# Kernel optimization log

Hardware: AMD Instinct MI355X
Metric: run time of the kernel (lower is better)

## Reference

```python
import jax, jax.numpy as jnp
import numpy as np

N = 200000
E = 200000
H = 256
NEG_INF = -1e30


def setup_inputs() -> dict:
    key = jax.random.key(0)
    k1, k2, k3, k4, k5, k6, k7 = jax.random.split(key, 7)
    node_tokens = jax.random.normal(k1, (N, H), dtype=jnp.float32)
    relation_tokens = jax.random.normal(k2, (E, H), dtype=jnp.float32)
    edge_index = jax.random.randint(k3, (2, E), 0, N, dtype=jnp.int64)
    node_is_cvt = jax.random.randint(k4, (N,), 0, 2) > 0
    # learned params (randomized for a non-trivial test; torch inits attn/shared to zeros)
    shared_cvt = jax.random.normal(k5, (H,), dtype=jnp.float32) * 0.02
    attn_vector = jax.random.normal(k6, (H,), dtype=jnp.float32) * 0.1
    W_msg = jax.random.normal(k7, (H, 2 * H), dtype=jnp.float32) * (1.0 / np.sqrt(2 * H))  # torch Linear weight [out,in]
    return {"node_tokens": node_tokens, "relation_tokens": relation_tokens,
            "edge_index": edge_index, "node_is_cvt": node_is_cvt,
            "shared_cvt": shared_cvt, "attn_vector": attn_vector, "W_msg": W_msg}


def reference(node_tokens, relation_tokens, edge_index, node_is_cvt, shared_cvt, attn_vector, W_msg):
    num_nodes, hidden = node_tokens.shape
    num_edges = relation_tokens.shape[0]
    tails = edge_index[1]                      # [E]
    cvt_mask = node_is_cvt.astype(bool)        # [N]
    edge_mask = cvt_mask[tails]                # [E] edges whose tail is a CVT node

    # faithful quirk: nbr token for edge i is node_tokens[i] (edge slot index)
    nbr = node_tokens[:num_edges]                                   # [E, H]
    msg = jnp.concatenate([relation_tokens, nbr], axis=-1) @ W_msg.T  # [E, H]

    # per-edge logits, segment-wise (per tail node) softmax over CVT-tail edges only
    logits = jnp.where(edge_mask, jnp.einsum('eh,h->e', msg, attn_vector), NEG_INF)
    m = jax.ops.segment_max(logits, tails, num_segments=num_nodes)   # [N]
    p = jnp.where(edge_mask, jnp.exp(logits - m[tails]), 0.0)        # [E]
    denom = jax.ops.segment_sum(p, tails, num_segments=num_nodes)    # [N]
    w = p / jnp.where(denom > 0, denom, 1.0)[tails]                  # [E]

    agg = jax.ops.segment_sum(msg * w[:, None], tails, num_segments=num_nodes)  # [N, H]
    cvt_tokens = agg + shared_cvt
    return jnp.where(cvt_mask[:, None], cvt_tokens, node_tokens)
```

## Files before the change

kernel.cpp:

```cpp
#include <hip/hip_runtime.h>
#include <math.h>

#define H   256
#define H2  512
#define MX  16

typedef __attribute__((ext_vector_type(4))) float f32x4;
typedef __attribute__((ext_vector_type(8))) short short8;

__device__ __forceinline__ short f2bf(float f) {
  unsigned u = __builtin_bit_cast(unsigned, f);
  u = (u + 0x7FFFu + ((u >> 16) & 1u)) >> 16;
  return (short)u;
}

__device__ __forceinline__ void gload_lds16(const void* g, void* l) {
  __builtin_amdgcn_global_load_lds(
      (const __attribute__((address_space(1))) unsigned int*)g,
      (__attribute__((address_space(3))) unsigned int*)l, 16, 0, 0);
}

__global__ void k_init(unsigned* cnt, int* ctrs, int N) {
  int i = blockIdx.x * blockDim.x + threadIdx.x;
  if (i < N) cnt[i] = 0u;
  if (i == 0) { ctrs[0] = 0; }
}

__global__ void k_prep(const int* __restrict__ ei, const int* __restrict__ cvt,
                       const float* __restrict__ W, const float* __restrict__ attn,
                       unsigned* __restrict__ cnt, int* __restrict__ ebuf,
                       float* __restrict__ u, short* __restrict__ Wt, int E) {
  int g = blockIdx.x * blockDim.x + threadIdx.x;
  if (g < E) {
    int tail = ei[E + g];
    if (cvt[tail]) {
      unsigned pos = atomicAdd(cnt + tail, 1u);
      if (pos < MX) ebuf[(size_t)tail * MX + pos] = g;
    }
  }
  if (g < 512) {
    float s = 0.f;
    for (int h = 0; h < H; ++h) s += W[(size_t)h * H2 + g] * attn[h];
    u[g] = s;
  }
  if (g < 16384) {
    int n = g & 255, kb = g >> 8;
    const float* src = W + (size_t)n * H2 + kb * 8;
    f32x4 a = *(const f32x4*)src;
    f32x4 b = *(const f32x4*)(src + 4);
    short8 o;
    o[0]=f2bf(a.x); o[1]=f2bf(a.y); o[2]=f2bf(a.z); o[3]=f2bf(a.w);
    o[4]=f2bf(b.x); o[5]=f2bf(b.y); o[6]=f2bf(b.z); o[7]=f2bf(b.w);
    *(short8*)(Wt + (size_t)(kb * 256 + n) * 8) = o;
  }
}

__global__ void k_slots(const unsigned* __restrict__ cnt, int* __restrict__ ctrs,
                        int* __restrict__ actpk, int N) {
  int n = blockIdx.x * blockDim.x + threadIdx.x;
  int lane = threadIdx.x & 63;
  unsigned c = (n < N) ? cnt[n] : 0u;
  bool active = c > 0u;
  unsigned long long mask = __ballot(active);
  if (!mask) return;
  int rank = __popcll(mask & ((1ull << lane) - 1ull));
  int wcount = __popcll(mask);
  int sbase = 0;
  if (lane == 0) sbase = atomicAdd(ctrs + 0, wcount);
  sbase = __shfl(sbase, 0);
  if (active) {
    int cc = (int)(c > MX ? MX : c);
    actpk[sbase + rank] = n | (cc << 20);
  }
}

__global__ __launch_bounds__(256) void k_fin(
    const float* __restrict__ NT, const int* __restrict__ cvt,
    const unsigned* __restrict__ cnt, const float* __restrict__ sc,
    const float* __restrict__ R, const float* __restrict__ u,
    const int* __restrict__ actpk, const int* __restrict__ ctrs,
    const int* __restrict__ ebuf, float* __restrict__ out, int N) {
  int wid = blockIdx.x * 4 + (threadIdx.x >> 6);
  int nw = gridDim.x * 4;
  int lane = threadIdx.x & 63;

  auto outinit = [&]() {
    f32x4 scl = ((const f32x4*)sc)[lane];
    for (int row = wid; row < N; row += nw) {
      int cv = cvt[row];
      if (cv && cnt[row] > 0u) continue;
      f32x4 v = cv ? scl : ((const f32x4*)NT)[(size_t)row * 64 + lane];
      ((f32x4*)out)[(size_t)row * 64 + lane] = v;
    }
  };

  auto gather = [&]() {
    int nAct = ctrs[0];
    int loff = lane * 8;
    const float* src0 = (loff < H) ? (R + loff) : (NT + (loff - H));
    const f32x4* u4 = (const f32x4*)u;
    f32x4 ua = u4[lane * 2], ub = u4[lane * 2 + 1];
    int s = wid;
    if (s >= nAct) return;
    int pk = actpk[s];
    int n = pk & 0xFFFFF, c = pk >> 20;
    int id = (lane < c) ? ebuf[(size_t)n * MX + lane] : 0;
    while (true) {
      int s2 = s + nw;
      int n2 = 0, c2 = 0, id2 = 0;
      if (s2 < nAct) {
        int pk2 = actpk[s2];
        n2 = pk2 & 0xFFFFF; c2 = pk2 >> 20;
        id2 = (lane < c2) ? ebuf[(size_t)n2 * MX + lane] : 0;
      }
      f32x4 x0, x1;
      if (c == 1) {
        int e = __shfl(id, 0);
        const f32x4* src = (const f32x4*)(src0 + (size_t)e * H);
        x0 = src[0]; x1 = src[1];
      } else if (c == 2) {
        int e0 = __shfl(id, 0), e1 = __shfl(id, 1);
        const f32x4* sA = (const f32x4*)(src0 + (size_t)e0 * H);
        const f32x4* sB = (const f32x4*)(src0 + (size_t)e1 * H);
        f32x4 a0 = sA[0], b0 = sA[1], a1 = sB[0], b1 = sB[1];
        float d0 = a0.x*ua.x + a0.y*ua.y + a0.z*ua.z + a0.w*ua.w
                 + b0.x*ub.x + b0.y*ub.y + b0.z*ub.z + b0.w*ub.w;
        float d1 = a1.x*ua.x + a1.y*ua.y + a1.z*ua.z + a1.w*ua.w
                 + b1.x*ub.x + b1.y*ub.y + b1.z*ub.z + b1.w*ub.w;
        #pragma unroll
        for (int off = 32; off > 0; off >>= 1) {
          d0 += __shfl_xor(d0, off);
          d1 += __shfl_xor(d1, off);
        }
        float p0 = __expf(d0), p1 = __expf(d1);
        float inv = 1.f / (p0 + p1);
        p0 *= inv; p1 *= inv;
        x0 = a0 * p0 + a1 * p1;
        x1 = b0 * p0 + b1 * p1;
      } else {
        x0 = (f32x4){0.f,0.f,0.f,0.f}; x1 = x0;
        float den = 0.f;
        for (int i = 0; i < c; ++i) {
          int e = __shfl(id, i);
          const f32x4* src = (const f32x4*)(src0 + (size_t)e * H);
          f32x4 a = src[0], b = src[1];
          float d = a.x*ua.x + a.y*ua.y + a.z*ua.z + a.w*ua.w
                  + b.x*ub.x + b.y*ub.y + b.z*ub.z + b.w*ub.w;
          #pragma unroll
          for (int off = 32; off > 0; off >>= 1) d += __shfl_xor(d, off);
          float pe = __expf(d);
          den += pe;
          x0 += a * pe;
          x1 += b * pe;
        }
        float inv = 1.f / den;
        x0 *= inv; x1 *= inv;
      }
      short8 o;
      o[0]=f2bf(x0.x); o[1]=f2bf(x0.y); o[2]=f2bf(x0.z); o[3]=f2bf(x0.w);
      o[4]=f2bf(x1.x); o[5]=f2bf(x1.y); o[6]=f2bf(x1.z); o[7]=f2bf(x1.w);
      *(short8*)((short*)(out + (size_t)n * H) + loff) = o;
      if (s2 >= nAct) break;
      s = s2; n = n2; c = c2; id = id2;
    }
  };

  if (wid & 1) { gather(); outinit(); }
  else         { outinit(); gather(); }
}

__global__ __launch_bounds__(256) void k_gemm2(
    const short* __restrict__ Wt, const int* __restrict__ actpk,
    const int* __restrict__ ctrs, const float* __restrict__ sc,
    float* __restrict__ out) {
  __shared__ __align__(16) short Bs[2][4][256][8];
  __shared__ __align__(16) short As[2][4][128][8];
  int nAct = ctrs[0];
  int base = blockIdx.x * 128;
  if (base >= nAct) return;
  int tid = threadIdx.x;
  int wave = tid >> 6, lane = tid & 63;
  int l15 = lane & 15, lg = lane >> 4;

  int slot0 = base + lane;       if (slot0 >= nAct) slot0 = nAct - 1;
  int slot1 = base + 64 + lane;  if (slot1 >= nAct) slot1 = nAct - 1;
  const short* arow0 = (const short*)(out + (size_t)(actpk[slot0] & 0xFFFFF) * H);
  const short* arow1 = (const short*)(out + (size_t)(actpk[slot1] & 0xFFFFF) * H);

  auto stage = [&](int b, int kk) {
    gload_lds16(arow0 + kk + wave * 8, &As[b][wave][0][0]);
    gload_lds16(arow1 + kk + wave * 8, &As[b][wave][64][0]);
    int kb = kk >> 3;
    #pragma unroll
    for (int it = 0; it < 4; ++it) {
      const short* src = Wt + (size_t)(kb + it) * 2048 + (size_t)tid * 8;
      gload_lds16(src, &Bs[b][it][wave * 64][0]);
    }
  };

  f32x4 acc[8][4];
  #pragma unroll
  for (int i = 0; i < 8; ++i)
    #pragma unroll
    for (int j = 0; j < 4; ++j) acc[i][j] = (f32x4){0.f, 0.f, 0.f, 0.f};

  stage(0, 0);
  __syncthreads();
  int cur = 0;
  for (int t = 0; t < 16; ++t) {
    if (t < 15) stage(cur ^ 1, (t + 1) * 32);
    short8 bf[4];
    #pragma unroll
    for (int ct = 0; ct < 4; ++ct)
      bf[ct] = *(const short8*)&Bs[cur][lg][wave * 64 + ct * 16 + l15][0];
    #pragma unroll
    for (int rt = 0; rt < 8; ++rt) {
      short8 af = *(const short8*)&As[cur][lg][rt * 16 + l15][0];
      #pragma unroll
      for (int ct = 0; ct < 4; ++ct)
        acc[rt][ct] = __builtin_amdgcn_mfma_f32_16x16x32_bf16(af, bf[ct], acc[rt][ct], 0, 0, 0);
    }
    __syncthreads();
    cur ^= 1;
  }

  #pragma unroll
  for (int rt = 0; rt < 8; ++rt) {
    #pragma unroll
    for (int rr = 0; rr < 4; ++rr) {
      int sD = base + rt * 16 + lg * 4 + rr;
      if (sD >= nAct) continue;
      int n = actpk[sD] & 0xFFFFF;
      float* orow = out + (size_t)n * H;
      #pragma unroll
      for (int ct = 0; ct < 4; ++ct) {
        int c = wave * 64 + ct * 16 + l15;
        __builtin_nontemporal_store(acc[rt][ct][rr] + sc[c], orow + c);
      }
    }
  }
}

extern "C" void kernel_launch(void* const* d_in, const int* in_sizes, int n_in,
                              void* d_out, int out_size, void* d_ws, size_t ws_size,
                              hipStream_t stream) {
  const float* NT   = (const float*)d_in[0];
  const float* R    = (const float*)d_in[1];
  const int*   ei   = (const int*)d_in[2];
  const int*   cvt  = (const int*)d_in[3];
  const float* sc   = (const float*)d_in[4];
  const float* attn = (const float*)d_in[5];
  const float* W    = (const float*)d_in[6];
  float* out = (float*)d_out;

  int N = in_sizes[0] / H;
  int E = in_sizes[1] / H;

  char* wsp = (char*)d_ws;
  auto alloc = [&](size_t bytes) { char* r = wsp; wsp += (bytes + 255) & ~(size_t)255; return r; };
  float*    u       = (float*)alloc(512 * 4);
  short*    Wt      = (short*)alloc((size_t)H * H2 * 2);
  int*      ebuf    = (int*)alloc((size_t)N * MX * 4);
  unsigned* cnt     = (unsigned*)alloc((size_t)N * 4);
  int*      actpk   = (int*)alloc((size_t)N * 4);
  int*      ctrs    = (int*)alloc(2 * 4);

  k_init<<<(N + 255) / 256, 256, 0, stream>>>(cnt, ctrs, N);
  k_prep<<<(E + 255) / 256, 256, 0, stream>>>(ei, cvt, W, attn, cnt, ebuf, u, Wt, E);
  k_slots<<<(N + 255) / 256, 256, 0, stream>>>(cnt, ctrs, actpk, N);
  k_fin<<<2048, 256, 0, stream>>>(NT, cvt, cnt, sc, R, u, actpk, ctrs, ebuf, out, N);
  k_gemm2<<<(N + 127) / 128, 256, 0, stream>>>(Wt, actpk, ctrs, sc, out);
}
```

Before: 208.8 us.

## Fuse attention gather into GEMM via LDS-resident swizzled A tiles

```diff
diff --git a/kernel.cpp b/kernel.cpp
--- a/kernel.cpp
+++ b/kernel.cpp
@@ -4,6 +4,7 @@
 #define H   256
 #define H2  512
 #define MX  16
+#define TR  32
 
 typedef __attribute__((ext_vector_type(4))) float f32x4;
 typedef __attribute__((ext_vector_type(8))) short short8;
@@ -74,148 +75,125 @@
   }
 }
 
-__global__ __launch_bounds__(256) void k_fin(
-    const float* __restrict__ NT, const int* __restrict__ cvt,
-    const unsigned* __restrict__ cnt, const float* __restrict__ sc,
-    const float* __restrict__ R, const float* __restrict__ u,
+__global__ __launch_bounds__(256) void k_gg(
+    const float* __restrict__ R, const float* __restrict__ NT,
+    const short* __restrict__ Wt, const float* __restrict__ u,
     const int* __restrict__ actpk, const int* __restrict__ ctrs,
-    const int* __restrict__ ebuf, float* __restrict__ out, int N) {
-  int wid = blockIdx.x * 4 + (threadIdx.x >> 6);
-  int nw = gridDim.x * 4;
-  int lane = threadIdx.x & 63;
-
-  auto outinit = [&]() {
-    f32x4 scl = ((const f32x4*)sc)[lane];
-    for (int row = wid; row < N; row += nw) {
-      int cv = cvt[row];
-      if (cv && cnt[row] > 0u) continue;
-      f32x4 v = cv ? scl : ((const f32x4*)NT)[(size_t)row * 64 + lane];
-      ((f32x4*)out)[(size_t)row * 64 + lane] = v;
+    const int* __restrict__ ebuf, const float* __restrict__ sc,
+    float* __restrict__ out) {
+  __shared__ __align__(16) short As[TR * 512];
+  __shared__ __align__(16) short Bs[2][4][256][8];
+  __shared__ int nIdx[TR];
+  int nAct = ctrs[0];
+  int base = blockIdx.x * TR;
+  if (base >= nAct) return;
+  int tid = threadIdx.x, wave = tid >> 6, lane = tid & 63;
+  int l15 = lane & 15, lg = lane >> 4;
+
+  auto stageB = [&](int b, int kk) {
+    int kb = kk >> 3;
+    #pragma unroll
+    for (int it = 0; it < 4; ++it) {
+      const short* src = Wt + (size_t)(kb + it) * 2048 + (size_t)tid * 8;
+      gload_lds16(src, &Bs[b][it][wave * 64][0]);
     }
   };
-
-  auto gather = [&]() {
-    int nAct = ctrs[0];
+  stageB(0, 0);
+
+  {
     int loff = lane * 8;
     const float* src0 = (loff < H) ? (R + loff) : (NT + (loff - H));
     const f32x4* u4 = (const f32x4*)u;
     f32x4 ua = u4[lane * 2], ub = u4[lane * 2 + 1];
-    int s = wid;
-    if (s >= nAct) return;
-    int pk = actpk[s];
-    int n = pk & 0xFFFFF, c = pk >> 20;
-    int id = (lane < c) ? ebuf[(size_t)n * MX + lane] : 0;
-    while (true) {
-      int s2 = s + nw;
-      int n2 = 0, c2 = 0, id2 = 0;
-      if (s2 < nAct) {
-        int pk2 = actpk[s2];
-        n2 = pk2 & 0xFFFFF; c2 = pk2 >> 20;
-        id2 = (lane < c2) ? ebuf[(size_t)n2 * MX + lane] : 0;
+    int s0 = base + wave * 8;
+    int nSlots = nAct - s0; if (nSlots > 8) nSlots = 8;
+    if (nSlots > 0) {
+      int myPk = (lane < nSlots) ? actpk[s0 + lane] : 0;
+      int pk = __shfl(myPk, 0);
+      int n = pk & 0xFFFFF, c = pk >> 20;
+      int id = (lane < c) ? ebuf[(size_t)n * MX + lane] : 0;
+      for (int i = 0; i < nSlots; ++i) {
+        int nN = 0, cN = 0, idN = 0;
+        if (i + 1 < nSlots) {
+          int pkN = __shfl(myPk, i + 1);
+          nN = pkN & 0xFFFFF; cN = pkN >> 20;
+          idN = (lane < cN) ? ebuf[(size_t)nN * MX + lane] : 0;
+        }
+        f32x4 x0, x1;
+        if (c == 1) {
+          int e = __shfl(id, 0);
+          const f32x4* src = (const f32x4*)(src0 + (size_t)e * H);
+          x0 = src[0]; x1 = src[1];
+        } else if (c == 2) {
+          int e0 = __shfl(id, 0), e1 = __shfl(id, 1);
+          const f32x4* sA = (const f32x4*)(src0 + (size_t)e0 * H);
+          const f32x4* sB = (const f32x4*)(src0 + (size_t)e1 * H);
+          f32x4 a0 = sA[0], b0 = sA[1], a1 = sB[0], b1 = sB[1];
+          float d0 = a0.x*ua.x + a0.y*ua.y + a0.z*ua.z + a0.w*ua.w
+                   + b0.x*ub.x + b0.y*ub.y + b0.z*ub.z + b0.w*ub.w;
+          float d1 = a1.x*ua.x + a1.y*ua.y + a1.z*ua.z + a1.w*ua.w
+                   + b1.x*ub.x + b1.y*ub.y + b1.z*ub.z + b1.w*ub.w;
+          #pragma unroll
+          for (int off = 32; off > 0; off >>= 1) {
+            d0 += __shfl_xor(d0, off);
+            d1 += __shfl_xor(d1, off);
+          }
+          float p0 = __expf(d0), p1 = __expf(d1);
+          float inv = 1.f / (p0 + p1);
+          p0 *= inv; p1 *= inv;
+          x0 = a0 * p0 + a1 * p1;
+          x1 = b0 * p0 + b1 * p1;
+        } else {
+          x0 = (f32x4){0.f,0.f,0.f,0.f}; x1 = x0;
+          float den = 0.f;
+          for (int j = 0; j < c; ++j) {
+            int e = __shfl(id, j);
+            const f32x4* src = (const f32x4*)(src0 + (size_t)e * H);
+            f32x4 a = src[0], b = src[1];
+            float d = a.x*ua.x + a.y*ua.y + a.z*ua.z + a.w*ua.w
+                    + b.x*ub.x + b.y*ub.y + b.z*ub.z + b.w*ub.w;
+            #pragma unroll
+            for (int off = 32; off > 0; off >>= 1) d += __shfl_xor(d, off);
+            float pe = __expf(d);
+            den += pe;
+            x0 += a * pe;
+            x1 += b * pe;
+          }
+          float inv = 1.f / den;
+          x0 *= inv; x1 *= inv;
+        }
+        short8 o;
+        o[0]=f2bf(x0.x); o[1]=f2bf(x0.y); o[2]=f2bf(x0.z); o[3]=f2bf(x0.w);
+        o[4]=f2bf(x1.x); o[5]=f2bf(x1.y); o[6]=f2bf(x1.z); o[7]=f2bf(x1.w);
+        int r = wave * 8 + i;
+        if (lane == 0) nIdx[r] = n;
+        char* dst = (char*)As + r * 1024 + ((lane * 16) ^ ((r & 7) << 4));
+        *(short8*)dst = o;
+        n = nN; c = cN; id = idN;
       }
-      f32x4 x0, x1;
-      if (c == 1) {
-        int e = __shfl(id, 0);
-        const f32x4* src = (const f32x4*)(src0 + (size_t)e * H);
-        x0 = src[0]; x1 = src[1];
-      } else if (c == 2) {
-        int e0 = __shfl(id, 0), e1 = __shfl(id, 1);
-        const f32x4* sA = (const f32x4*)(src0 + (size_t)e0 * H);
-        const f32x4* sB = (const f32x4*)(src0 + (size_t)e1 * H);
-        f32x4 a0 = sA[0], b0 = sA[1], a1 = sB[0], b1 = sB[1];
-        float d0 = a0.x*ua.x + a0.y*ua.y + a0.z*ua.z + a0.w*ua.w
-                 + b0.x*ub.x + b0.y*ub.y + b0.z*ub.z + b0.w*ub.w;
-        float d1 = a1.x*ua.x + a1.y*ua.y + a1.z*ua.z + a1.w*ua.w
-                 + b1.x*ub.x + b1.y*ub.y + b1.z*ub.z + b1.w*ub.w;
-        #pragma unroll
-        for (int off = 32; off > 0; off >>= 1) {
-          d0 += __shfl_xor(d0, off);
-          d1 += __shfl_xor(d1, off);
-        }
-        float p0 = __expf(d0), p1 = __expf(d1);
-        float inv = 1.f / (p0 + p1);
-        p0 *= inv; p1 *= inv;
-        x0 = a0 * p0 + a1 * p1;
-        x1 = b0 * p0 + b1 * p1;
-      } else {
-        x0 = (f32x4){0.f,0.f,0.f,0.f}; x1 = x0;
-        float den = 0.f;
-        for (int i = 0; i < c; ++i) {
-          int e = __shfl(id, i);
-          const f32x4* src = (const f32x4*)(src0 + (size_t)e * H);
-          f32x4 a = src[0], b = src[1];
-          float d = a.x*ua.x + a.y*ua.y + a.z*ua.z + a.w*ua.w
-                  + b.x*ub.x + b.y*ub.y + b.z*ub.z + b.w*ub.w;
-          #pragma unroll
-          for (int off = 32; off > 0; off >>= 1) d += __shfl_xor(d, off);
-          float pe = __expf(d);
-          den += pe;
-          x0 += a * pe;
-          x1 += b * pe;
-        }
-        float inv = 1.f / den;
-        x0 *= inv; x1 *= inv;
-      }
-      short8 o;
-      o[0]=f2bf(x0.x); o[1]=f2bf(x0.y); o[2]=f2bf(x0.z); o[3]=f2bf(x0.w);
-      o[4]=f2bf(x1.x); o[5]=f2bf(x1.y); o[6]=f2bf(x1.z); o[7]=f2bf(x1.w);
-      *(short8*)((short*)(out + (size_t)n * H) + loff) = o;
-      if (s2 >= nAct) break;
-      s = s2; n = n2; c = c2; id = id2;
-    }
-  };
-
-  if (wid & 1) { gather(); outinit(); }
-  else         { outinit(); gather(); }
-}
-
-__global__ __launch_bounds__(256) void k_gemm2(
-    const short* __restrict__ Wt, const int* __restrict__ actpk,
-    const int* __restrict__ ctrs, const float* __restrict__ sc,
-    float* __restrict__ out) {
-  __shared__ __align__(16) short Bs[2][4][256][8];
-  __shared__ __align__(16) short As[2][4][128][8];
-  int nAct = ctrs[0];
-  int base = blockIdx.x * 128;
-  if (base >= nAct) return;
-  int tid = threadIdx.x;
-  int wave = tid >> 6, lane = tid & 63;
-  int l15 = lane & 15, lg = lane >> 4;
-
-  int slot0 = base + lane;       if (slot0 >= nAct) slot0 = nAct - 1;
-  int slot1 = base + 64 + lane;  if (slot1 >= nAct) slot1 = nAct - 1;
-  const short* arow0 = (const short*)(out + (size_t)(actpk[slot0] & 0xFFFFF) * H);
-  const short* arow1 = (const short*)(out + (size_t)(actpk[slot1] & 0xFFFFF) * H);
-
-  auto stage = [&](int b, int kk) {
-    gload_lds16(arow0 + kk + wave * 8, &As[b][wave][0][0]);
-    gload_lds16(arow1 + kk + wave * 8, &As[b][wave][64][0]);
-    int kb = kk >> 3;
-    #pragma unroll
-    for (int it = 0; it < 4; ++it) {
-      const short* src = Wt + (size_t)(kb + it) * 2048 + (size_t)tid * 8;
-      gload_lds16(src, &Bs[b][it][wave * 64][0]);
-    }
-  };
-
-  f32x4 acc[8][4];
+    }
+  }
+  __syncthreads();
+
+  f32x4 acc[2][4];
   #pragma unroll
-  for (int i = 0; i < 8; ++i)
+  for (int i = 0; i < 2; ++i)
     #pragma unroll
     for (int j = 0; j < 4; ++j) acc[i][j] = (f32x4){0.f, 0.f, 0.f, 0.f};
 
-  stage(0, 0);
-  __syncthreads();
   int cur = 0;
   for (int t = 0; t < 16; ++t) {
-    if (t < 15) stage(cur ^ 1, (t + 1) * 32);
+    if (t < 15) stageB(cur ^ 1, (t + 1) * 32);
+    int kk = t * 32;
     short8 bf[4];
     #pragma unroll
     for (int ct = 0; ct < 4; ++ct)
       bf[ct] = *(const short8*)&Bs[cur][lg][wave * 64 + ct * 16 + l15][0];
     #pragma unroll
-    for (int rt = 0; rt < 8; ++rt) {
-      short8 af = *(const short8*)&As[cur][lg][rt * 16 + l15][0];
+    for (int rt = 0; rt < 2; ++rt) {
+      int row = rt * 16 + l15;
+      short8 af = *(const short8*)((const char*)As + row * 1024 +
+                                   (((kk + lg * 8) * 2) ^ ((row & 7) << 4)));
       #pragma unroll
       for (int ct = 0; ct < 4; ++ct)
         acc[rt][ct] = __builtin_amdgcn_mfma_f32_16x16x32_bf16(af, bf[ct], acc[rt][ct], 0, 0, 0);
@@ -225,12 +203,12 @@
   }
 
   #pragma unroll
-  for (int rt = 0; rt < 8; ++rt) {
+  for (int rt = 0; rt < 2; ++rt) {
     #pragma unroll
     for (int rr = 0; rr < 4; ++rr) {
-      int sD = base + rt * 16 + lg * 4 + rr;
-      if (sD >= nAct) continue;
-      int n = actpk[sD] & 0xFFFFF;
+      int lrow = rt * 16 + lg * 4 + rr;
+      if (base + lrow >= nAct) continue;
+      int n = nIdx[lrow];
       float* orow = out + (size_t)n * H;
       #pragma unroll
       for (int ct = 0; ct < 4; ++ct) {
@@ -238,6 +216,22 @@
         __builtin_nontemporal_store(acc[rt][ct][rr] + sc[c], orow + c);
       }
     }
+  }
+}
+
+__global__ __launch_bounds__(256) void k_out(
+    const float* __restrict__ NT, const int* __restrict__ cvt,
+    const unsigned* __restrict__ cnt, const float* __restrict__ sc,
+    float* __restrict__ out, int N) {
+  int wid = blockIdx.x * 4 + (threadIdx.x >> 6);
+  int nw = gridDim.x * 4;
+  int lane = threadIdx.x & 63;
+  f32x4 scl = ((const f32x4*)sc)[lane];
+  for (int row = wid; row < N; row += nw) {
+    int cv = cvt[row];
+    if (cv && cnt[row] > 0u) continue;
+    f32x4 v = cv ? scl : ((const f32x4*)NT)[(size_t)row * 64 + lane];
+    ((f32x4*)out)[(size_t)row * 64 + lane] = v;
   }
 }
 
@@ -268,6 +262,6 @@
   k_init<<<(N + 255) / 256, 256, 0, stream>>>(cnt, ctrs, N);
   k_prep<<<(E + 255) / 256, 256, 0, stream>>>(ei, cvt, W, attn, cnt, ebuf, u, Wt, E);
   k_slots<<<(N + 255) / 256, 256, 0, stream>>>(cnt, ctrs, actpk, N);
-  k_fin<<<2048, 256, 0, stream>>>(NT, cvt, cnt, sc, R, u, actpk, ctrs, ebuf, out, N);
-  k_gemm2<<<(N + 127) / 128, 256, 0, stream>>>(Wt, actpk, ctrs, sc, out);
-}
+  k_gg<<<(N + TR - 1) / TR, 256, 0, stream>>>(R, NT, Wt, u, actpk, ctrs, ebuf, sc, out);
+  k_out<<<2048, 256, 0, stream>>>(NT, cvt, cnt, sc, out, N);
+}
```

Result: slower. 235.6 us (+12.8%).

## Move output-init pass from gather kernel into GEMM kernel as extra blocks

Applied to the files above, without the earlier changes.

```diff
diff --git a/kernel.cpp b/kernel.cpp
--- a/kernel.cpp
+++ b/kernel.cpp
@@ -74,17 +74,98 @@
   }
 }
 
-__global__ __launch_bounds__(256) void k_fin(
-    const float* __restrict__ NT, const int* __restrict__ cvt,
-    const unsigned* __restrict__ cnt, const float* __restrict__ sc,
-    const float* __restrict__ R, const float* __restrict__ u,
-    const int* __restrict__ actpk, const int* __restrict__ ctrs,
-    const int* __restrict__ ebuf, float* __restrict__ out, int N) {
+__global__ __launch_bounds__(256) void k_gather(
+    const float* __restrict__ R, const float* __restrict__ NT,
+    const float* __restrict__ u, const int* __restrict__ actpk,
+    const int* __restrict__ ctrs, const int* __restrict__ ebuf,
+    float* __restrict__ out) {
+  int nAct = ctrs[0];
   int wid = blockIdx.x * 4 + (threadIdx.x >> 6);
   int nw = gridDim.x * 4;
   int lane = threadIdx.x & 63;
-
-  auto outinit = [&]() {
+  int loff = lane * 8;
+  const float* src0 = (loff < H) ? (R + loff) : (NT + (loff - H));
+  const f32x4* u4 = (const f32x4*)u;
+  f32x4 ua = u4[lane * 2], ub = u4[lane * 2 + 1];
+  int s = wid;
+  if (s >= nAct) return;
+  int pk = actpk[s];
+  int n = pk & 0xFFFFF, c = pk >> 20;
+  int id = (lane < c) ? ebuf[(size_t)n * MX + lane] : 0;
+  while (true) {
+    int s2 = s + nw;
+    int n2 = 0, c2 = 0, id2 = 0;
+    if (s2 < nAct) {
+      int pk2 = actpk[s2];
+      n2 = pk2 & 0xFFFFF; c2 = pk2 >> 20;
+      id2 = (lane < c2) ? ebuf[(size_t)n2 * MX + lane] : 0;
+    }
+    f32x4 x0, x1;
+    if (c == 1) {
+      int e = __shfl(id, 0);
+      const f32x4* src = (const f32x4*)(src0 + (size_t)e * H);
+      x0 = src[0]; x1 = src[1];
+    } else if (c == 2) {
+      int e0 = __shfl(id, 0), e1 = __shfl(id, 1);
+      const f32x4* sA = (const f32x4*)(src0 + (size_t)e0 * H);
+      const f32x4* sB = (const f32x4*)(src0 + (size_t)e1 * H);
+      f32x4 a0 = sA[0], b0 = sA[1], a1 = sB[0], b1 = sB[1];
+      float d0 = a0.x*ua.x + a0.y*ua.y + a0.z*ua.z + a0.w*ua.w
+               + b0.x*ub.x + b0.y*ub.y + b0.z*ub.z + b0.w*ub.w;
+      float d1 = a1.x*ua.x + a1.y*ua.y + a1.z*ua.z + a1.w*ua.w
+               + b1.x*ub.x + b1.y*ub.y + b1.z*ub.z + b1.w*ub.w;
+      #pragma unroll
+      for (int off = 32; off > 0; off >>= 1) {
+        d0 += __shfl_xor(d0, off);
+        d1 += __shfl_xor(d1, off);
+      }
+      float p0 = __expf(d0), p1 = __expf(d1);
+      float inv = 1.f / (p0 + p1);
+      p0 *= inv; p1 *= inv;
+      x0 = a0 * p0 + a1 * p1;
+      x1 = b0 * p0 + b1 * p1;
+    } else {
+      x0 = (f32x4){0.f,0.f,0.f,0.f}; x1 = x0;
+      float den = 0.f;
+      for (int i = 0; i < c; ++i) {
+        int e = __shfl(id, i);
+        const f32x4* src = (const f32x4*)(src0 + (size_t)e * H);
+        f32x4 a = src[0], b = src[1];
+        float d = a.x*ua.x + a.y*ua.y + a.z*ua.z + a.w*ua.w
+                + b.x*ub.x + b.y*ub.y + b.z*ub.z + b.w*ub.w;
+        #pragma unroll
+        for (int off = 32; off > 0; off >>= 1) d += __shfl_xor(d, off);
+        float pe = __expf(d);
+        den += pe;
+        x0 += a * pe;
+        x1 += b * pe;
+      }
+      float inv = 1.f / den;
+      x0 *= inv; x1 *= inv;
+    }
+    short8 o;
+    o[0]=f2bf(x0.x); o[1]=f2bf(x0.y); o[2]=f2bf(x0.z); o[3]=f2bf(x0.w);
+    o[4]=f2bf(x1.x); o[5]=f2bf(x1.y); o[6]=f2bf(x1.z); o[7]=f2bf(x1.w);
+    *(short8*)((short*)(out + (size_t)n * H) + loff) = o;
+    if (s2 >= nAct) break;
+    s = s2; n = n2; c = c2; id = id2;
+  }
+}
+
+__global__ __launch_bounds__(256) void k_go(
+    const short* __restrict__ Wt, const int* __restrict__ actpk,
+    const int* __restrict__ ctrs, const float* __restrict__ sc,
+    const float* __restrict__ NT, const int* __restrict__ cvt,
+    const unsigned* __restrict__ cnt, float* __restrict__ out,
+    int N, int G, int OUTB) {
+  __shared__ __align__(16) short Bs[2][4][256][8];
+  __shared__ __align__(16) short As[2][4][128][8];
+  int tid = threadIdx.x;
+  int wave = tid >> 6, lane = tid & 63;
+
+  if ((int)blockIdx.x >= G) {
+    int wid = ((int)blockIdx.x - G) * 4 + wave;
+    int nw = OUTB * 4;
     f32x4 scl = ((const f32x4*)sc)[lane];
     for (int row = wid; row < N; row += nw) {
       int cv = cvt[row];
@@ -92,94 +173,12 @@
       f32x4 v = cv ? scl : ((const f32x4*)NT)[(size_t)row * 64 + lane];
       ((f32x4*)out)[(size_t)row * 64 + lane] = v;
     }
-  };
-
-  auto gather = [&]() {
-    int nAct = ctrs[0];
-    int loff = lane * 8;
-    const float* src0 = (loff < H) ? (R + loff) : (NT + (loff - H));
-    const f32x4* u4 = (const f32x4*)u;
-    f32x4 ua = u4[lane * 2], ub = u4[lane * 2 + 1];
-    int s = wid;
-    if (s >= nAct) return;
-    int pk = actpk[s];
-    int n = pk & 0xFFFFF, c = pk >> 20;
-    int id = (lane < c) ? ebuf[(size_t)n * MX + lane] : 0;
-    while (true) {
-      int s2 = s + nw;
-      int n2 = 0, c2 = 0, id2 = 0;
-      if (s2 < nAct) {
-        int pk2 = actpk[s2];
-        n2 = pk2 & 0xFFFFF; c2 = pk2 >> 20;
-        id2 = (lane < c2) ? ebuf[(size_t)n2 * MX + lane] : 0;
-      }
-      f32x4 x0, x1;
-      if (c == 1) {
-        int e = __shfl(id, 0);
-        const f32x4* src = (const f32x4*)(src0 + (size_t)e * H);
-        x0 = src[0]; x1 = src[1];
-      } else if (c == 2) {
-        int e0 = __shfl(id, 0), e1 = __shfl(id, 1);
-        const f32x4* sA = (const f32x4*)(src0 + (size_t)e0 * H);
-        const f32x4* sB = (const f32x4*)(src0 + (size_t)e1 * H);
-        f32x4 a0 = sA[0], b0 = sA[1], a1 = sB[0], b1 = sB[1];
-        float d0 = a0.x*ua.x + a0.y*ua.y + a0.z*ua.z + a0.w*ua.w
-                 + b0.x*ub.x + b0.y*ub.y + b0.z*ub.z + b0.w*ub.w;
-        float d1 = a1.x*ua.x + a1.y*ua.y + a1.z*ua.z + a1.w*ua.w
-                 + b1.x*ub.x + b1.y*ub.y + b1.z*ub.z + b1.w*ub.w;
-        #pragma unroll
-        for (int off = 32; off > 0; off >>= 1) {
-          d0 += __shfl_xor(d0, off);
-          d1 += __shfl_xor(d1, off);
-        }
-        float p0 = __expf(d0), p1 = __expf(d1);
-        float inv = 1.f / (p0 + p1);
-        p0 *= inv; p1 *= inv;
-        x0 = a0 * p0 + a1 * p1;
-        x1 = b0 * p0 + b1 * p1;
-      } else {
-        x0 = (f32x4){0.f,0.f,0.f,0.f}; x1 = x0;
-        float den = 0.f;
-        for (int i = 0; i < c; ++i) {
-          int e = __shfl(id, i);
-          const f32x4* src = (const f32x4*)(src0 + (size_t)e * H);
-          f32x4 a = src[0], b = src[1];
-          float d = a.x*ua.x + a.y*ua.y + a.z*ua.z + a.w*ua.w
-                  + b.x*ub.x + b.y*ub.y + b.z*ub.z + b.w*ub.w;
-          #pragma unroll
-          for (int off = 32; off > 0; off >>= 1) d += __shfl_xor(d, off);
-          float pe = __expf(d);
-          den += pe;
-          x0 += a * pe;
-          x1 += b * pe;
-        }
-        float inv = 1.f / den;
-        x0 *= inv; x1 *= inv;
-      }
-      short8 o;
-      o[0]=f2bf(x0.x); o[1]=f2bf(x0.y); o[2]=f2bf(x0.z); o[3]=f2bf(x0.w);
-      o[4]=f2bf(x1.x); o[5]=f2bf(x1.y); o[6]=f2bf(x1.z); o[7]=f2bf(x1.w);
-      *(short8*)((short*)(out + (size_t)n * H) + loff) = o;
-      if (s2 >= nAct) break;
-      s = s2; n = n2; c = c2; id = id2;
-    }
-  };
-
-  if (wid & 1) { gather(); outinit(); }
-  else         { outinit(); gather(); }
-}
-
-__global__ __launch_bounds__(256) void k_gemm2(
-    const short* __restrict__ Wt, const int* __restrict__ actpk,
-    const int* __restrict__ ctrs, const float* __restrict__ sc,
-    float* __restrict__ out) {
-  __shared__ __align__(16) short Bs[2][4][256][8];
-  __shared__ __align__(16) short As[2][4][128][8];
+    return;
+  }
+
   int nAct = ctrs[0];
   int base = blockIdx.x * 128;
   if (base >= nAct) return;
-  int tid = threadIdx.x;
-  int wave = tid >> 6, lane = tid & 63;
   int l15 = lane & 15, lg = lane >> 4;
 
   int slot0 = base + lane;       if (slot0 >= nAct) slot0 = nAct - 1;
@@ -265,9 +264,12 @@
   int*      actpk   = (int*)alloc((size_t)N * 4);
   int*      ctrs    = (int*)alloc(2 * 4);
 
+  int G = (N + 127) / 128;
+  int OUTB = 1024;
+
   k_init<<<(N + 255) / 256, 256, 0, stream>>>(cnt, ctrs, N);
   k_prep<<<(E + 255) / 256, 256, 0, stream>>>(ei, cvt, W, attn, cnt, ebuf, u, Wt, E);
   k_slots<<<(N + 255) / 256, 256, 0, stream>>>(cnt, ctrs, actpk, N);
-  k_fin<<<2048, 256, 0, stream>>>(NT, cvt, cnt, sc, R, u, actpk, ctrs, ebuf, out, N);
-  k_gemm2<<<(N + 127) / 128, 256, 0, stream>>>(Wt, actpk, ctrs, sc, out);
-}
+  k_gather<<<2048, 256, 0, stream>>>(R, NT, u, actpk, ctrs, ebuf, out);
+  k_go<<<G + OUTB, 256, 0, stream>>>(Wt, actpk, ctrs, sc, NT, cvt, cnt, out, N, G, OUTB);
+}
```

Result: slower. 263.0 us (+25.9%).
